# Optimization experiments

Measured on AMD Instinct MI355X. Metric: run time of the kernel, lower is better.

The kernel has to match this reference:

```python
import jax, jax.numpy as jnp
import numpy as np

VOCAB = 32000
D = 768          # embed_size
SEQ = 2048       # seq_len (max_len for positional table)
B = 16
PAD = 0
SEG_VOCAB = 3


def make_pe(d_model, max_len):
    # Faithful to the (nonstandard) loop: for even i: sin(pos/10000**(2i/d)),
    # at i+1: cos(pos/10000**(2(i+1)/d)).
    pos = np.arange(max_len, dtype=np.float32)[:, None]           # [L,1]
    i = np.arange(0, d_model, 2, dtype=np.float32)[None, :]       # [1,D/2]
    pe = np.zeros((max_len, d_model), dtype=np.float32)
    pe[:, 0::2] = np.sin(pos / 10000.0 ** (2.0 * i / d_model))
    pe[:, 1::2] = np.cos(pos / 10000.0 ** (2.0 * (i + 1.0) / d_model))
    return jnp.asarray(pe)[None]  # [1, L, D]


def semantic_embed(ids, W, b, padding_idx):
    # one_hot(ids) @ W.T + b  ==  gather column of W (row of W.T) + b
    emb = jnp.take(W.T, ids, axis=0) + b                 # [B,S,D]
    is_pad = ids == padding_idx                          # [B,S]
    pad_vec = jnp.full((W.shape[0],), float(padding_idx), dtype=emb.dtype)
    # Original: where(attention_mask.unsqueeze(-1) == 0, padding_embedding, embeddings)
    # i.e. NON-pad tokens get the constant padding vector, pad tokens keep emb.
    return jnp.where(is_pad[..., None], emb, pad_vec)


def setup_inputs() -> dict:
    key = jax.random.key(0)
    k1, k2, k3, k4, k5, k6 = jax.random.split(key, 6)
    input_ids = jax.random.randint(k1, (B, SEQ), 0, VOCAB, dtype=jnp.int64)
    segment_label = jax.random.randint(k2, (B, SEQ), 0, SEG_VOCAB, dtype=jnp.int64)
    W_tok = jax.random.normal(k3, (D, VOCAB), dtype=jnp.float32) * 0.02
    b_tok = jax.random.normal(k4, (D,), dtype=jnp.float32) * 0.02
    W_seg = jax.random.normal(k5, (D, SEG_VOCAB), dtype=jnp.float32) * 0.02
    b_seg = jax.random.normal(k6, (D,), dtype=jnp.float32) * 0.02
    pe = make_pe(D, SEQ)
    return {"input_ids": input_ids, "segment_label": segment_label,
            "W_tok": W_tok, "b_tok": b_tok, "W_seg": W_seg, "b_seg": b_seg,
            "pe": pe}


def reference(input_ids, segment_label, W_tok, b_tok, W_seg, b_seg, pe):
    S = input_ids.shape[1]
    tok = semantic_embed(input_ids, W_tok, b_tok, PAD)      # [B,S,D]
    seg = semantic_embed(segment_label, W_seg, b_seg, PAD)  # [B,S,D]
    x = tok + pe[:, :S, :] + seg
    # dropout is identity in eval mode
    return x
```

## Files before the change

kernel.cpp:

```cpp
#include <hip/hip_runtime.h>


#define VOCAB 32000
#define DMODEL 768
#define SEQ 2048
#define NB 16
#define D4 (DMODEL / 4)

__global__ void precompute_vecs(const float* __restrict__ W_tok,
                                const float* __restrict__ b_tok,
                                const float* __restrict__ W_seg,
                                const float* __restrict__ b_seg,
                                float* __restrict__ v) {
    int d = blockIdx.x * blockDim.x + threadIdx.x;
    if (d < DMODEL) {
        v[d]          = W_tok[(size_t)d * VOCAB] + b_tok[d];
        v[DMODEL + d] = W_seg[d * 3] + b_seg[d];
    }
}

__global__ __launch_bounds__(192) void embed_kernel(
        const int* __restrict__ ids,
        const int* __restrict__ segs,
        const float* __restrict__ pe,
        const float* __restrict__ v,
        float* __restrict__ out) {
    const int row = blockIdx.x;
    const int s = row & (SEQ - 1);
    const int d4 = threadIdx.x;

    const bool t = (ids[row] == 0);
    const bool g = (segs[row] == 0);

    const float4* pe4 = (const float4*)pe;
    const float4* vt4 = (const float4*)v;
    const float4* vg4 = (const float4*)(v + DMODEL);

    float4 p  = pe4[s * D4 + d4];
    float4 vt = vt4[d4];
    float4 vg = vg4[d4];

    float4 o;
    o.x = ((t ? vt.x : 0.0f) + p.x) + (g ? vg.x : 0.0f);
    o.y = ((t ? vt.y : 0.0f) + p.y) + (g ? vg.y : 0.0f);
    o.z = ((t ? vt.z : 0.0f) + p.z) + (g ? vg.z : 0.0f);
    o.w = ((t ? vt.w : 0.0f) + p.w) + (g ? vg.w : 0.0f);

    ((float4*)out)[(size_t)row * D4 + d4] = o;
}

extern "C" void kernel_launch(void* const* d_in, const int* in_sizes, int n_in,
                              void* d_out, int out_size, void* d_ws, size_t ws_size,
                              hipStream_t stream) {
    const int*   ids   = (const int*)d_in[0];
    const int*   segs  = (const int*)d_in[1];
    const float* W_tok = (const float*)d_in[2];
    const float* b_tok = (const float*)d_in[3];
    const float* W_seg = (const float*)d_in[4];
    const float* b_seg = (const float*)d_in[5];
    const float* pe    = (const float*)d_in[6];
    float* out = (float*)d_out;
    float* v   = (float*)d_ws;

    precompute_vecs<<<3, 256, 0, stream>>>(W_tok, b_tok, W_seg, b_seg, v);
    embed_kernel<<<NB * SEQ, 192, 0, stream>>>(ids, segs, pe, v, out);
}
```

Before: 180.9 us.

## Process all batches per sequence position and use nontemporal stores

Each block now handles one sequence position for all 16 batch entries, so each positional-encoding row and the two bias vectors are loaded once and reused across the batch instead of reloaded per row. The grid shrinks from 32768 to 2048 blocks, and output writes use nontemporal stores to avoid polluting cache. The risks are lower parallelism with fewer blocks, 16 scattered id/segment loads per thread, and more registers.

```diff
diff --git a/kernel.cpp b/kernel.cpp
--- a/kernel.cpp
+++ b/kernel.cpp
@@ -6,6 +6,8 @@
 #define SEQ 2048
 #define NB 16
 #define D4 (DMODEL / 4)
+
+typedef float f4 __attribute__((ext_vector_type(4)));
 
 __global__ void precompute_vecs(const float* __restrict__ W_tok,
                                 const float* __restrict__ b_tok,
@@ -25,28 +27,27 @@
         const float* __restrict__ pe,
         const float* __restrict__ v,
         float* __restrict__ out) {
-    const int row = blockIdx.x;
-    const int s = row & (SEQ - 1);
+    const int s  = blockIdx.x;
     const int d4 = threadIdx.x;
 
-    const bool t = (ids[row] == 0);
-    const bool g = (segs[row] == 0);
+    const f4 p  = ((const f4*)pe)[s * D4 + d4];
+    const f4 vt = ((const f4*)v)[d4];
+    const f4 vg = ((const f4*)(v + DMODEL))[d4];
+    const f4 zero = {0.0f, 0.0f, 0.0f, 0.0f};
 
-    const float4* pe4 = (const float4*)pe;
-    const float4* vt4 = (const float4*)v;
-    const float4* vg4 = (const float4*)(v + DMODEL);
+    bool t[NB], g[NB];
+#pragma unroll
+    for (int b = 0; b < NB; ++b) {
+        t[b] = (ids[b * SEQ + s] == 0);
+        g[b] = (segs[b * SEQ + s] == 0);
+    }
 
-    float4 p  = pe4[s * D4 + d4];
-    float4 vt = vt4[d4];
-    float4 vg = vg4[d4];
-
-    float4 o;
-    o.x = ((t ? vt.x : 0.0f) + p.x) + (g ? vg.x : 0.0f);
-    o.y = ((t ? vt.y : 0.0f) + p.y) + (g ? vg.y : 0.0f);
-    o.z = ((t ? vt.z : 0.0f) + p.z) + (g ? vg.z : 0.0f);
-    o.w = ((t ? vt.w : 0.0f) + p.w) + (g ? vg.w : 0.0f);
-
-    ((float4*)out)[(size_t)row * D4 + d4] = o;
+    f4* o4 = (f4*)out;
+#pragma unroll
+    for (int b = 0; b < NB; ++b) {
+        f4 o = ((t[b] ? vt : zero) + p) + (g[b] ? vg : zero);
+        __builtin_nontemporal_store(o, &o4[((size_t)b * SEQ + s) * D4 + d4]);
+    }
 }
 
 extern "C" void kernel_launch(void* const* d_in, const int* in_sizes, int n_in,
@@ -63,5 +64,5 @@
     float* v   = (float*)d_ws;
 
     precompute_vecs<<<3, 256, 0, stream>>>(W_tok, b_tok, W_seg, b_seg, v);
-    embed_kernel<<<NB * SEQ, 192, 0, stream>>>(ids, segs, pe, v, out);
+    embed_kernel<<<SEQ, 192, 0, stream>>>(ids, segs, pe, v, out);
 }
```

New measurement: 173.7 us. 4.0% less time.
